# Kernel optimization log

Measured on AMD Instinct MI355X. Metric: run time of the kernel, lower is better.

## Reference

```python
import jax, jax.numpy as jnp
import numpy as np

N, D_IN, D_LAT, D_FEAT, K = 12000, 64, 16, 64, 16


def setup_inputs() -> dict:
    key = jax.random.key(0)
    ks = jax.random.split(key, 7)
    s_in = 1.0 / np.sqrt(D_IN)
    s_cat = 1.0 / np.sqrt(2 * D_FEAT)
    return {
        "x": jax.random.normal(ks[0], (N, D_IN), dtype=jnp.float32),
        "W_feat": jax.random.uniform(ks[1], (D_IN, D_FEAT), jnp.float32, -s_in, s_in),
        "b_feat": jax.random.uniform(ks[2], (D_FEAT,), jnp.float32, -s_in, s_in),
        "W_lat": jax.random.uniform(ks[3], (D_IN, D_LAT), jnp.float32, -s_in, s_in),
        "b_lat": jax.random.uniform(ks[4], (D_LAT,), jnp.float32, -s_in, s_in),
        "W_out": jax.random.uniform(ks[5], (2 * D_FEAT, D_FEAT), jnp.float32, -s_cat, s_cat),
        "b_out": jax.random.uniform(ks[6], (D_FEAT,), jnp.float32, -s_cat, s_cat),
    }


def reference(x, W_feat, b_feat, W_lat, b_lat, W_out, b_out):
    # dense encoders
    feats = jnp.tanh(x @ W_feat + b_feat)      # [N, F] learned features
    coords = jnp.tanh(x @ W_lat + b_lat)       # [N, S] latent coordinates
    n = coords.shape[0]
    # full pairwise squared euclidean distances (as the module's cdist)
    sq = jnp.sum(coords * coords, axis=1)
    d2 = sq[:, None] + sq[None, :] - 2.0 * (coords @ coords.T)   # [N, N]
    d2 = jnp.maximum(d2, 0.0)
    # knn_graph: k nearest neighbors, excluding self (loop=False)
    d2_masked = jnp.where(jnp.eye(n, dtype=bool), jnp.inf, d2)
    neg_d2, idx = jax.lax.top_k(-d2_masked, K)                   # idx: [N, K] neighbor (source) ids
    edge_d2 = -neg_d2                                            # squared dist to each neighbor
    # gaussian kernel on euclidean distance: w = exp(-d^2)
    w = jnp.exp(-edge_d2)                                        # [N, K]
    # message = w * x_j, aggr='add': out_i = sum_k w_ik * feats[idx_ik]
    agg = jnp.einsum('nk,nkf->nf', w, feats[idx])                # [N, F]
    # cat self features with aggregated messages, final dense
    out = jnp.concatenate([feats, agg], axis=1) @ W_out + b_out  # [N, F]
    return out
```

## Files before the change

### kernel.cpp

```cpp
#include <hip/hip_runtime.h>
#include <math.h>

typedef unsigned long long u64;
typedef _Float16 f16x8 __attribute__((ext_vector_type(8)));
typedef float f32x16 __attribute__((ext_vector_type(16)));

#define N_PTS 12000
#define KNN 16
#define QB 16
#define NWAVES 8
#define NGROUPS32 (N_PTS / 32)
#define TAU_PTS 4096
#define TAU_GROUPS32 (TAU_PTS / 32)
#define CAP 384
#define MARGIN 0.08f
#define EVICT_KEY ((u64)0x7F400000u << 32)

__global__ __launch_bounds__(256) void encoder_kernel(
    const float* __restrict__ x, const float* __restrict__ Wf, const float* __restrict__ bf,
    const float* __restrict__ Wl, const float* __restrict__ bl,
    float* __restrict__ feats, float* __restrict__ coords, _Float16* __restrict__ coords_h,
    float* __restrict__ sq)
{
  const int wave = threadIdx.x >> 6;
  const int lane = threadIdx.x & 63;
  const int i = blockIdx.x * 4 + wave;
  if (i >= N_PTS) return;
  float xv = x[i * 64 + lane];
  float accf0 = bf[lane], accf1 = 0.0f;
  float accc0 = bl[lane & 15], accc1 = 0.0f;
  #pragma unroll
  for (int k = 0; k < 64; k += 2) {
    const float xk0 = __shfl(xv, k);
    const float xk1 = __shfl(xv, k + 1);
    accf0 = fmaf(xk0, Wf[k * 64 + lane], accf0);
    accf1 = fmaf(xk1, Wf[(k + 1) * 64 + lane], accf1);
    accc0 = fmaf(xk0, Wl[k * 16 + (lane & 15)], accc0);
    accc1 = fmaf(xk1, Wl[(k + 1) * 16 + (lane & 15)], accc1);
  }
  feats[i * 64 + lane] = tanhf(accf0 + accf1);
  float c = tanhf(accc0 + accc1);
  float cc = (lane < 16) ? c * c : 0.0f;
  cc += __shfl_xor(cc, 1);
  cc += __shfl_xor(cc, 2);
  cc += __shfl_xor(cc, 4);
  cc += __shfl_xor(cc, 8);
  if (lane < 16) {
    coords[i * 16 + lane] = c;
    coords_h[i * 16 + lane] = (_Float16)c;
  }
  if (lane == 0) sq[i] = cc;
}

__device__ __forceinline__ void ins6(u64 key, u64* k6, u64& kmax) {
  const u64 om = (key < kmax) ? kmax : ~0ull;
  #pragma unroll
  for (int t = 0; t < 6; ++t)
    k6[t] = (k6[t] == om) ? key : k6[t];
  u64 a = k6[0] > k6[1] ? k6[0] : k6[1];
  u64 b = k6[2] > k6[3] ? k6[2] : k6[3];
  u64 c = k6[4] > k6[5] ? k6[4] : k6[5];
  a = a > b ? a : b;
  kmax = a > c ? a : c;
}

__device__ __forceinline__ void ins8(u64 key, u64* k8, u64& kmax) {
  const u64 om = (key < kmax) ? kmax : ~0ull;
  #pragma unroll
  for (int t = 0; t < 8; ++t)
    k8[t] = (k8[t] == om) ? key : k8[t];
  u64 a = k8[0] > k8[1] ? k8[0] : k8[1];
  u64 b = k8[2] > k8[3] ? k8[2] : k8[3];
  u64 c = k8[4] > k8[5] ? k8[4] : k8[5];
  u64 d = k8[6] > k8[7] ? k8[6] : k8[7];
  a = a > b ? a : b;
  c = c > d ? c : d;
  kmax = a > c ? a : c;
}

__device__ __forceinline__ u64 shflx_u64(u64 v, int off) {
  int lo = __shfl_xor((int)(unsigned)v, off);
  int hi = __shfl_xor((int)(unsigned)(v >> 32), off);
  return ((u64)(unsigned)hi << 32) | (unsigned)lo;
}

__device__ __forceinline__ u64 minbfly(u64 m) {
  #pragma unroll
  for (int off = 32; off >= 1; off >>= 1) {
    u64 o = shflx_u64(m, off);
    m = (o < m) ? o : m;
  }
  return m;
}

#define CAS6(i, j) { const u64 a_ = k6[i], b_ = k6[j]; const bool sw_ = a_ > b_; \
                     k6[i] = sw_ ? b_ : a_; k6[j] = sw_ ? a_ : b_; }

#define LOADG(g, uu, ss) { const int jl_ = (g) * 32 + mcol; \
  uu = *(const uint4*)((const char*)coords_h + (size_t)jl_ * 32 + half * 16); \
  ss = sq[jl_]; }

__global__ __launch_bounds__(512, 6) void knn_agg_kernel(
    const float* __restrict__ coords, const _Float16* __restrict__ coords_h,
    const float* __restrict__ sq, const float* __restrict__ feats,
    const float* __restrict__ Wo, const float* __restrict__ bo,
    float* __restrict__ out, int* __restrict__ flags)
{
  __shared__ unsigned short sbuf[QB][CAP];
  __shared__ int scnt[QB];
  __shared__ unsigned colminS[QB][64];
  __shared__ float taugS[QB];
  __shared__ u64 keyS[QB][KNN];
  __shared__ __align__(16) float featS[QB][64];
  __shared__ __align__(16) float aggS[QB][64];

  const int tid = threadIdx.x;
  const int lane = tid & 63;
  const int wave = tid >> 6;
  const int qbase = blockIdx.x * QB;
  const int mcol = lane & 31;
  const int half = lane >> 5;

  if (tid < QB) scnt[tid] = 0;
  #pragma unroll
  for (int t = tid; t < QB * 64; t += 512)
    ((unsigned*)colminS)[t] = 0x7F800000u;

  f16x8 afrag = {0, 0, 0, 0, 0, 0, 0, 0};
  if (mcol < QB) {
    const uint4 u = *(const uint4*)((const char*)coords_h + (qbase + mcol) * 32 + half * 16);
    afrag = __builtin_bit_cast(f16x8, u);
  }
  float nhsqi8[8];
  #pragma unroll
  for (int blk = 0; blk < 2; ++blk) {
    const float4 v = *(const float4*)&sq[qbase + blk * 8 + 4 * half];
    nhsqi8[blk * 4 + 0] = -0.5f * v.x; nhsqi8[blk * 4 + 1] = -0.5f * v.y;
    nhsqi8[blk * 4 + 2] = -0.5f * v.z; nhsqi8[blk * 4 + 3] = -0.5f * v.w;
  }

  f32x16 acc;
  #pragma unroll
  for (int t = 0; t < 16; ++t) acc[t] = 0.0f;

  __syncthreads();

  const int g_self = qbase >> 5;
  float lmax8[8] = {-INFINITY, -INFINITY, -INFINITY, -INFINITY,
                    -INFINITY, -INFINITY, -INFINITY, -INFINITY};
  {
    uint4 pu0, pu1, pu2; float ps0, ps1, ps2;
    LOADG(wave,                pu0, ps0);
    LOADG(wave + NWAVES,       pu1, ps1);
    LOADG(wave + 2 * NWAVES,   pu2, ps2);
    for (int k = 0; k < 16; ++k) {
      const int g = wave + k * NWAVES;
      const uint4 cu = pu0; const float cs = ps0;
      pu0 = pu1; ps0 = ps1; pu1 = pu2; ps1 = ps2;
      const int kn = k + 3;
      const int gs = (kn < 16) ? (wave + kn * NWAVES) : wave;
      LOADG(gs, pu2, ps2);

      const f16x8 bfrag = __builtin_bit_cast(f16x8, cu);
      #pragma unroll
      for (int r = 0; r < 8; ++r) acc[r] = fmaf(-0.5f, cs, nhsqi8[r]);
      acc = __builtin_amdgcn_mfma_f32_32x32x16_f16(afrag, bfrag, acc, 0, 0, 0);
      if (g == g_self) {
        #pragma unroll
        for (int r = 0; r < 8; ++r) {
          const int row = (r >> 2) * 8 + 4 * half + (r & 3);
          if (g * 32 + mcol == qbase + row) acc[r] = -INFINITY;
        }
      }
      #pragma unroll
      for (int r = 0; r < 8; ++r) lmax8[r] = fmaxf(lmax8[r], acc[r]);
    }
  }
  {
    const int cell = mcol * 2 + (wave >> 2);
    #pragma unroll
    for (int r = 0; r < 8; ++r) {
      const int row = (r >> 2) * 8 + 4 * half + (r & 3);
      atomicMin(&colminS[row][cell], __float_as_uint(fmaxf(-2.0f * lmax8[r], 0.0f)));
    }
  }
  __syncthreads();

  #pragma unroll
  for (int s = 0; s < 2; ++s) {
    const int q = wave * 2 + s;
    float v = __uint_as_float(colminS[q][lane]);
    #pragma unroll
    for (int k = 2; k <= 64; k <<= 1) {
      #pragma unroll
      for (int st = k >> 1; st >= 1; st >>= 1) {
        const float o = __shfl_xor(v, st);
        const bool keepMin = (((lane & st) == 0) == ((lane & k) == 0));
        const float mn = fminf(v, o), mx = fmaxf(v, o);
        v = keepMin ? mn : mx;
      }
    }
    const float tq = __shfl(v, 15) + MARGIN;
    if (lane == 0) taugS[q] = tq;
  }
  __syncthreads();

  float nht8[8];
  #pragma unroll
  for (int r = 0; r < 8; ++r)
    nht8[r] = -0.5f * taugS[(r >> 2) * 8 + 4 * half + (r & 3)];

  {
    uint4 pu0, pu1, pu2; float ps0, ps1, ps2;
    LOADG(wave,                pu0, ps0);
    LOADG(wave + NWAVES,       pu1, ps1);
    LOADG(wave + 2 * NWAVES,   pu2, ps2);
    for (int g = wave; g < NGROUPS32; g += NWAVES) {
      const uint4 cu = pu0; const float cs = ps0;
      pu0 = pu1; ps0 = ps1; pu1 = pu2; ps1 = ps2;
      const int gn = g + 3 * NWAVES;
      const int gs = (gn < NGROUPS32) ? gn : wave;
      LOADG(gs, pu2, ps2);

      const f16x8 bfrag = __builtin_bit_cast(f16x8, cu);
      #pragma unroll
      for (int r = 0; r < 8; ++r) acc[r] = fmaf(-0.5f, cs, nhsqi8[r]);
      acc = __builtin_amdgcn_mfma_f32_32x32x16_f16(afrag, bfrag, acc, 0, 0, 0);
      const int j0 = g * 32;
      #pragma unroll
      for (int r = 0; r < 8; ++r) {
        if (acc[r] >= nht8[r]) {
          const int row = (r >> 2) * 8 + 4 * half + (r & 3);
          const int p = atomicAdd(&scnt[row], 1);
          if (p < CAP) sbuf[row][p] = (unsigned short)(j0 + mcol);
        }
      }
    }
  }
  __syncthreads();

  const int h = lane >> 5;
  u64 Al[6], Bl[6];

  #pragma unroll
  for (int s = 0; s < 2; ++s) {
    const int lq = wave * 2 + s;
    const int qg = qbase + lq;
    const int cq = scnt[lq];
    const int nread = (cq < CAP) ? cq : CAP;
    const int nit = (nread + 63) >> 6;

    float ci[16];
    {
      const float4* cp = (const float4*)(coords + qg * 16);
      *(float4*)&ci[0] = cp[0]; *(float4*)&ci[4] = cp[1];
      *(float4*)&ci[8] = cp[2]; *(float4*)&ci[12] = cp[3];
    }
    const float sqiq = sq[qg];

    u64 k6[6];
    #pragma unroll
    for (int t = 0; t < 6; ++t) k6[t] = ((u64)(0x7F000000u + t) << 32);
    u64 kmax6 = ((u64)0x7F000005u << 32);

    for (int t = 0; t < nit; ++t) {
      const int idx = t * 64 + lane;
      u64 key = ~0ull;
      if (idx < nread) {
        const int jj = sbuf[lq][idx];
        if (jj != qg) {
          const float4* cp = (const float4*)(coords + jj * 16);
          float dot = 0.0f;
          {
            const float4 c0 = cp[0], c1 = cp[1];
            dot = fmaf(ci[0], c0.x, dot); dot = fmaf(ci[1], c0.y, dot);
            dot = fmaf(ci[2], c0.z, dot); dot = fmaf(ci[3], c0.w, dot);
            dot = fmaf(ci[4], c1.x, dot); dot = fmaf(ci[5], c1.y, dot);
            dot = fmaf(ci[6], c1.z, dot); dot = fmaf(ci[7], c1.w, dot);
          }
          {
            const float4 c2 = cp[2], c3 = cp[3];
            dot = fmaf(ci[8],  c2.x, dot); dot = fmaf(ci[9],  c2.y, dot);
            dot = fmaf(ci[10], c2.z, dot); dot = fmaf(ci[11], c2.w, dot);
            dot = fmaf(ci[12], c3.x, dot); dot = fmaf(ci[13], c3.y, dot);
            dot = fmaf(ci[14], c3.z, dot); dot = fmaf(ci[15], c3.w, dot);
          }
          const float d2 = fmaxf(fmaf(-2.0f, dot, sqiq + sq[jj]), 0.0f);
          key = ((u64)__float_as_uint(d2) << 32) | (unsigned)jj;
        }
      }
      ins6(key, k6, kmax6);
    }

    CAS6(0,5) CAS6(1,3) CAS6(2,4)
    CAS6(1,2) CAS6(3,4)
    CAS6(0,3) CAS6(2,5)
    CAS6(0,1) CAS6(2,3) CAS6(4,5)
    CAS6(1,2) CAS6(3,4)

    #pragma unroll
    for (int t = 0; t < 6; ++t) {
      const u64 p = shflx_u64(k6[t], 32);
      if (h == s) { Al[t] = k6[t]; Bl[t] = p; }
    }
    if (lane == 0) flags[qg] = (cq > CAP);
  }

  {
    u64 myhead = (Al[0] < Bl[0]) ? Al[0] : Bl[0];
    #pragma unroll
    for (int r = 0; r < KNN; ++r) {
      u64 m = myhead;
      #pragma unroll
      for (int off = 16; off >= 1; off >>= 1) {
        const u64 o = shflx_u64(m, off);
        m = (o < m) ? o : m;
      }
      if ((lane & 31) == 0) keyS[wave * 2 + h][r] = m;
      const bool me = (myhead == m);
      const bool fa = me && (Al[0] == m);
      const bool fb = me && !fa;
      Al[0] = fa ? Al[1] : Al[0]; Al[1] = fa ? Al[2] : Al[1];
      Al[2] = fa ? Al[3] : Al[2]; Al[3] = fa ? Al[4] : Al[3];
      Al[4] = fa ? Al[5] : Al[4]; Al[5] = fa ? EVICT_KEY : Al[5];
      Bl[0] = fb ? Bl[1] : Bl[0]; Bl[1] = fb ? Bl[2] : Bl[1];
      Bl[2] = fb ? Bl[3] : Bl[2]; Bl[3] = fb ? Bl[4] : Bl[3];
      Bl[4] = fb ? Bl[5] : Bl[4]; Bl[5] = fb ? EVICT_KEY : Bl[5];
      myhead = (Al[0] < Bl[0]) ? Al[0] : Bl[0];
    }
  }

  #pragma unroll
  for (int s = 0; s < 2; ++s) {
    const int lq = wave * 2 + s;
    const int qg = qbase + lq;
    float aggv = 0.0f;
    #pragma unroll
    for (int r = 0; r < KNN; ++r) {
      const u64 m = keyS[lq][r];
      const float w = __expf(-__uint_as_float((unsigned)(m >> 32)));
      const int jj = (int)(unsigned)(m & 0xFFFFFFFFull);
      aggv = fmaf(w, feats[jj * 64 + lane], aggv);
    }
    aggS[lq][lane] = aggv;
    featS[lq][lane] = feats[qg * 64 + lane];
  }

  __syncthreads();
  const int row = tid >> 5;
  const int c2 = (tid & 31) * 2;
  float acc0 = bo[c2], acc1 = bo[c2 + 1];
  #pragma unroll
  for (int f0 = 0; f0 < 64; f0 += 4) {
    const float4 fv = *(const float4*)&featS[row][f0];
    const float4 av = *(const float4*)&aggS[row][f0];
    #pragma unroll
    for (int u = 0; u < 4; ++u) {
      const float fvu = (u == 0) ? fv.x : (u == 1) ? fv.y : (u == 2) ? fv.z : fv.w;
      const float avu = (u == 0) ? av.x : (u == 1) ? av.y : (u == 2) ? av.z : av.w;
      const float2 w0 = *(const float2*)&Wo[(f0 + u) * 64 + c2];
      const float2 w1 = *(const float2*)&Wo[(64 + f0 + u) * 64 + c2];
      acc0 = fmaf(fvu, w0.x, acc0); acc0 = fmaf(avu, w1.x, acc0);
      acc1 = fmaf(fvu, w0.y, acc1); acc1 = fmaf(avu, w1.y, acc1);
    }
  }
  const int orow = qbase + row;
  *(float2*)&out[orow * 64 + c2] = make_float2(acc0, acc1);
}

__global__ __launch_bounds__(256) void knn_fixup_kernel(
    const float* __restrict__ coords, const float* __restrict__ sq,
    const float* __restrict__ feats, const int* __restrict__ flags,
    const float* __restrict__ Wo, const float* __restrict__ bo,
    float* __restrict__ out)
{
  const int wave = threadIdx.x >> 6;
  const int lane = threadIdx.x & 63;
  const int i = blockIdx.x * 4 + wave;
  if (i >= N_PTS) return;
  if (!flags[i]) return;
  float ci[16];
  #pragma unroll
  for (int d = 0; d < 16; ++d) ci[d] = coords[i * 16 + d];
  const float sqi = sq[i];

  u64 k8a[8], k8b[8], kmaxA, kmaxB;
  #pragma unroll
  for (int t = 0; t < 8; ++t) {
    k8a[t] = ((u64)(0x7F000000u + t) << 32);
    k8b[t] = ((u64)(0x7F000000u + t) << 32);
  }
  kmaxA = ((u64)0x7F000007u << 32);
  kmaxB = ((u64)0x7F000007u << 32);

  const int niter = (N_PTS + 63) / 64;
  for (int t = 0; t < niter; ++t) {
    const int j = t * 64 + lane;
    float4 c0 = make_float4(0,0,0,0), c1 = c0, c2 = c0, c3 = c0;
    float sqj = 0.0f;
    if (j < N_PTS) {
      const float4* cp = (const float4*)(coords + j * 16);
      c0 = cp[0]; c1 = cp[1]; c2 = cp[2]; c3 = cp[3];
      sqj = sq[j];
    }
    float dot = ci[0]*c0.x + ci[1]*c0.y + ci[2]*c0.z + ci[3]*c0.w
              + ci[4]*c1.x + ci[5]*c1.y + ci[6]*c1.z + ci[7]*c1.w
              + ci[8]*c2.x + ci[9]*c2.y + ci[10]*c2.z + ci[11]*c2.w
              + ci[12]*c3.x + ci[13]*c3.y + ci[14]*c3.z + ci[15]*c3.w;
    float d2 = fmaxf(fmaf(-2.0f, dot, sqi + sqj), 0.0f);
    const unsigned hi = (j == i || j >= N_PTS) ? 0xFFFFFFFFu : __float_as_uint(d2);
    const u64 key = ((u64)hi << 32) | (unsigned)j;
    if (t & 1) ins8(key, k8a, kmaxA);
    else       ins8(key, k8b, kmaxB);
  }

  u64 tab[16];
  #pragma unroll
  for (int t = 0; t < 8; ++t) { tab[t] = k8a[t]; tab[8 + t] = k8b[t]; }
  u64 lmin = tab[0];
  #pragma unroll
  for (int t = 1; t < 16; ++t) lmin = (tab[t] < lmin) ? tab[t] : lmin;

  float aggv = 0.0f;
  u64 T16 = 0;
  for (int r = 0; r < KNN; ++r) {
    const u64 m = minbfly(lmin);
    if (lmin == m) {
      #pragma unroll
      for (int t = 0; t < 16; ++t) tab[t] = (tab[t] == m) ? ~0ull : tab[t];
      lmin = tab[0];
      #pragma unroll
      for (int t = 1; t < 16; ++t) lmin = (tab[t] < lmin) ? tab[t] : lmin;
    }
    const unsigned hi = (unsigned)(m >> 32);
    const bool ok = hi < 0x7F000000u;
    const float w = ok ? expf(-__uint_as_float(hi)) : 0.0f;
    const int jj = ok ? (int)(unsigned)(m & 0xFFFFFFFFull) : 0;
    aggv = fmaf(w, feats[jj * 64 + lane], aggv);
    T16 = m;
  }

  if (__any((kmaxA < T16) || (kmaxB < T16))) {
    aggv = 0.0f;
    u64 prev = 0;
    for (int r = 0; r < KNN; ++r) {
      u64 best = ~0ull;
      for (int j = lane; j < N_PTS; j += 64) {
        float dot = 0.0f;
        #pragma unroll
        for (int d = 0; d < 16; ++d) dot = fmaf(ci[d], coords[j * 16 + d], dot);
        const float d2 = fmaxf(fmaf(-2.0f, dot, sqi + sq[j]), 0.0f);
        const unsigned hi = (j == i) ? 0xFFFFFFFFu : __float_as_uint(d2);
        const u64 key = ((u64)hi << 32) | (unsigned)j;
        const bool cand = (r == 0) || (key > prev);
        if (cand && key < best) best = key;
      }
      const u64 m = minbfly(best);
      prev = m;
      const unsigned hi = (unsigned)(m >> 32);
      const bool ok = hi < 0x7F000000u;
      const float w = ok ? expf(-__uint_as_float(hi)) : 0.0f;
      const int jj = ok ? (int)(unsigned)(m & 0xFFFFFFFFull) : 0;
      aggv = fmaf(w, feats[jj * 64 + lane], aggv);
    }
  }

  const float fl = feats[i * 64 + lane];
  float acc = bo[lane];
  #pragma unroll
  for (int f = 0; f < 64; ++f) {
    acc = fmaf(__shfl(fl, f),   Wo[f * 64 + lane],        acc);
    acc = fmaf(__shfl(aggv, f), Wo[(64 + f) * 64 + lane], acc);
  }
  out[i * 64 + lane] = acc;
}

extern "C" void kernel_launch(void* const* d_in, const int* in_sizes, int n_in,
                              void* d_out, int out_size, void* d_ws, size_t ws_size,
                              hipStream_t stream) {
  const float* x  = (const float*)d_in[0];
  const float* Wf = (const float*)d_in[1];
  const float* bf = (const float*)d_in[2];
  const float* Wl = (const float*)d_in[3];
  const float* bl = (const float*)d_in[4];
  const float* Wo = (const float*)d_in[5];
  const float* bo = (const float*)d_in[6];
  float* out = (float*)d_out;

  char* ws = (char*)d_ws;
  float*     feats    = (float*)(ws);
  float*     coords   = (float*)(ws + 3072000);
  float*     sqv      = (float*)(ws + 3840000);
  _Float16*  coords_h = (_Float16*)(ws + 3888000);
  int*       flags    = (int*)(ws + 4272000);

  encoder_kernel<<<3000, 256, 0, stream>>>(x, Wf, bf, Wl, bl, feats, coords, coords_h, sqv);
  knn_agg_kernel<<<N_PTS / QB, 512, 0, stream>>>(coords, coords_h, sqv, feats, Wo, bo, out, flags);
  knn_fixup_kernel<<<3000, 256, 0, stream>>>(coords, sqv, feats, flags, Wo, bo, out);
}
```

Baseline: 172.2 us.

## Simplify kNN merge via wave-wide ballot selection, shallower prefetch, persistent fixup grid

Reduces the distance-scan prefetch from three groups ahead to one, which cuts register pressure. It replaces the half-wave A/B list merge through shared keyS with a per-query 64-lane min reduction, using ballot and readlane to pick the owner. The fixup kernel becomes a grid-stride loop over 47 blocks instead of 3000 mostly-idle blocks. The shallower prefetch risks exposing more memory latency, and the per-query full-wave reduction adds shuffle work.

Result: slower. 183.9 us (+6.8%).

```diff
diff --git a/kernel.cpp b/kernel.cpp
--- a/kernel.cpp
+++ b/kernel.cpp
@@ -110,7 +110,6 @@
   __shared__ int scnt[QB];
   __shared__ unsigned colminS[QB][64];
   __shared__ float taugS[QB];
-  __shared__ u64 keyS[QB][KNN];
   __shared__ __align__(16) float featS[QB][64];
   __shared__ __align__(16) float aggS[QB][64];
 
@@ -149,17 +148,13 @@
   float lmax8[8] = {-INFINITY, -INFINITY, -INFINITY, -INFINITY,
                     -INFINITY, -INFINITY, -INFINITY, -INFINITY};
   {
-    uint4 pu0, pu1, pu2; float ps0, ps1, ps2;
-    LOADG(wave,                pu0, ps0);
-    LOADG(wave + NWAVES,       pu1, ps1);
-    LOADG(wave + 2 * NWAVES,   pu2, ps2);
+    uint4 pu; float ps;
+    LOADG(wave, pu, ps);
     for (int k = 0; k < 16; ++k) {
       const int g = wave + k * NWAVES;
-      const uint4 cu = pu0; const float cs = ps0;
-      pu0 = pu1; ps0 = ps1; pu1 = pu2; ps1 = ps2;
-      const int kn = k + 3;
-      const int gs = (kn < 16) ? (wave + kn * NWAVES) : wave;
-      LOADG(gs, pu2, ps2);
+      const uint4 cu = pu; const float cs = ps;
+      const int kn = (k + 1 < 16) ? (k + 1) : 0;
+      LOADG(wave + kn * NWAVES, pu, ps);
 
       const f16x8 bfrag = __builtin_bit_cast(f16x8, cu);
       #pragma unroll
@@ -211,16 +206,13 @@
     nht8[r] = -0.5f * taugS[(r >> 2) * 8 + 4 * half + (r & 3)];
 
   {
-    uint4 pu0, pu1, pu2; float ps0, ps1, ps2;
-    LOADG(wave,                pu0, ps0);
-    LOADG(wave + NWAVES,       pu1, ps1);
-    LOADG(wave + 2 * NWAVES,   pu2, ps2);
+    uint4 pu; float ps;
+    LOADG(wave, pu, ps);
     for (int g = wave; g < NGROUPS32; g += NWAVES) {
-      const uint4 cu = pu0; const float cs = ps0;
-      pu0 = pu1; ps0 = ps1; pu1 = pu2; ps1 = ps2;
-      const int gn = g + 3 * NWAVES;
-      const int gs = (gn < NGROUPS32) ? gn : wave;
-      LOADG(gs, pu2, ps2);
+      const uint4 cu = pu; const float cs = ps;
+      int gn = g + NWAVES;
+      if (gn >= NGROUPS32) gn = wave;
+      LOADG(gn, pu, ps);
 
       const f16x8 bfrag = __builtin_bit_cast(f16x8, cu);
       #pragma unroll
@@ -238,9 +230,6 @@
     }
   }
   __syncthreads();
-
-  const int h = lane >> 5;
-  u64 Al[6], Bl[6];
 
   #pragma unroll
   for (int s = 0; s < 2; ++s) {
@@ -298,52 +287,39 @@
     CAS6(0,1) CAS6(2,3) CAS6(4,5)
     CAS6(1,2) CAS6(3,4)
 
-    #pragma unroll
-    for (int t = 0; t < 6; ++t) {
-      const u64 p = shflx_u64(k6[t], 32);
-      if (h == s) { Al[t] = k6[t]; Bl[t] = p; }
-    }
-    if (lane == 0) flags[qg] = (cq > CAP);
-  }
-
-  {
-    u64 myhead = (Al[0] < Bl[0]) ? Al[0] : Bl[0];
+    float dmin = __uint_as_float((unsigned)(k6[0] >> 32));
+    int jmin = (int)(unsigned)(k6[0] & 0xFFFFFFFFull);
+
+    float dv[16]; int jv[16];
     #pragma unroll
     for (int r = 0; r < KNN; ++r) {
-      u64 m = myhead;
-      #pragma unroll
-      for (int off = 16; off >= 1; off >>= 1) {
-        const u64 o = shflx_u64(m, off);
-        m = (o < m) ? o : m;
-      }
-      if ((lane & 31) == 0) keyS[wave * 2 + h][r] = m;
-      const bool me = (myhead == m);
-      const bool fa = me && (Al[0] == m);
-      const bool fb = me && !fa;
-      Al[0] = fa ? Al[1] : Al[0]; Al[1] = fa ? Al[2] : Al[1];
-      Al[2] = fa ? Al[3] : Al[2]; Al[3] = fa ? Al[4] : Al[3];
-      Al[4] = fa ? Al[5] : Al[4]; Al[5] = fa ? EVICT_KEY : Al[5];
-      Bl[0] = fb ? Bl[1] : Bl[0]; Bl[1] = fb ? Bl[2] : Bl[1];
-      Bl[2] = fb ? Bl[3] : Bl[2]; Bl[3] = fb ? Bl[4] : Bl[3];
-      Bl[4] = fb ? Bl[5] : Bl[4]; Bl[5] = fb ? EVICT_KEY : Bl[5];
-      myhead = (Al[0] < Bl[0]) ? Al[0] : Bl[0];
-    }
-  }
-
-  #pragma unroll
-  for (int s = 0; s < 2; ++s) {
-    const int lq = wave * 2 + s;
-    const int qg = qbase + lq;
+      float m = dmin;
+      #pragma unroll
+      for (int off = 32; off >= 1; off >>= 1)
+        m = fminf(m, __shfl_xor(m, off));
+      const u64 bal = __ballot(dmin == m);
+      const int owner = __ffsll((unsigned long long)bal) - 1;
+      jv[r] = __builtin_amdgcn_readlane(jmin, owner);
+      dv[r] = __uint_as_float(__builtin_amdgcn_readfirstlane(__float_as_uint(m)));
+      const bool me = (lane == owner);
+      k6[0] = me ? k6[1] : k6[0];
+      k6[1] = me ? k6[2] : k6[1];
+      k6[2] = me ? k6[3] : k6[2];
+      k6[3] = me ? k6[4] : k6[3];
+      k6[4] = me ? k6[5] : k6[4];
+      k6[5] = me ? EVICT_KEY : k6[5];
+      dmin = __uint_as_float((unsigned)(k6[0] >> 32));
+      jmin = (int)(unsigned)(k6[0] & 0xFFFFFFFFull);
+    }
+
     float aggv = 0.0f;
     #pragma unroll
-    for (int r = 0; r < KNN; ++r) {
-      const u64 m = keyS[lq][r];
-      const float w = __expf(-__uint_as_float((unsigned)(m >> 32)));
-      const int jj = (int)(unsigned)(m & 0xFFFFFFFFull);
-      aggv = fmaf(w, feats[jj * 64 + lane], aggv);
-    }
+    for (int r = 0; r < KNN; ++r)
+      aggv = fmaf(__expf(-dv[r]), feats[jv[r] * 64 + lane], aggv);
+
     aggS[lq][lane] = aggv;
     featS[lq][lane] = feats[qg * 64 + lane];
+    if (lane == 0) flags[qg] = (cq > CAP);
   }
 
   __syncthreads();
@@ -376,9 +352,8 @@
 {
   const int wave = threadIdx.x >> 6;
   const int lane = threadIdx.x & 63;
-  const int i = blockIdx.x * 4 + wave;
-  if (i >= N_PTS) return;
-  if (!flags[i]) return;
+  for (int i = blockIdx.x * 4 + wave; i < N_PTS; i += 188) {
+  if (!flags[i]) continue;
   float ci[16];
   #pragma unroll
   for (int d = 0; d < 16; ++d) ci[d] = coords[i * 16 + d];
@@ -466,13 +441,14 @@
   }
 
   const float fl = feats[i * 64 + lane];
-  float acc = bo[lane];
+  float accv = bo[lane];
   #pragma unroll
   for (int f = 0; f < 64; ++f) {
-    acc = fmaf(__shfl(fl, f),   Wo[f * 64 + lane],        acc);
-    acc = fmaf(__shfl(aggv, f), Wo[(64 + f) * 64 + lane], acc);
-  }
-  out[i * 64 + lane] = acc;
+    accv = fmaf(__shfl(fl, f),   Wo[f * 64 + lane],        accv);
+    accv = fmaf(__shfl(aggv, f), Wo[(64 + f) * 64 + lane], accv);
+  }
+  out[i * 64 + lane] = accv;
+  }
 }
 
 extern "C" void kernel_launch(void* const* d_in, const int* in_sizes, int n_in,
@@ -496,5 +472,5 @@
 
   encoder_kernel<<<3000, 256, 0, stream>>>(x, Wf, bf, Wl, bl, feats, coords, coords_h, sqv);
   knn_agg_kernel<<<N_PTS / QB, 512, 0, stream>>>(coords, coords_h, sqv, feats, Wo, bo, out, flags);
-  knn_fixup_kernel<<<3000, 256, 0, stream>>>(coords, sqv, feats, flags, Wo, bo, out);
-}
+  knn_fixup_kernel<<<47, 256, 0, stream>>>(coords, sqv, feats, flags, Wo, bo, out);
+}
```
